# Kernel tuning notes

Hardware: AMD Instinct MI355X
Metric: run time of the kernel (lower is better)

The kernel has to match this reference:

```python
import jax, jax.numpy as jnp
import numpy as np

D_MODEL = 1024
NUM_HEADS = 16
D_K = D_MODEL // NUM_HEADS


def setup_inputs() -> dict:
    key = jax.random.key(0)
    ks = jax.random.split(key, 9)
    s = 1.0 / np.sqrt(D_MODEL)
    return {
        "z": jax.random.normal(ks[0], (4, 2048, D_MODEL), dtype=jnp.float32),
        "Wq": jax.random.uniform(ks[1], (D_MODEL, D_MODEL), jnp.float32, -s, s),
        "bq": jax.random.uniform(ks[2], (D_MODEL,), jnp.float32, -s, s),
        "Wk": jax.random.uniform(ks[3], (D_MODEL, D_MODEL), jnp.float32, -s, s),
        "bk": jax.random.uniform(ks[4], (D_MODEL,), jnp.float32, -s, s),
        "Wv": jax.random.uniform(ks[5], (D_MODEL, D_MODEL), jnp.float32, -s, s),
        "bv": jax.random.uniform(ks[6], (D_MODEL,), jnp.float32, -s, s),
        "Wo": jax.random.uniform(ks[7], (D_MODEL, D_MODEL), jnp.float32, -s, s),
        "bo": jax.random.uniform(ks[8], (D_MODEL,), jnp.float32, -s, s),
    }


def reference(z, Wq, bq, Wk, bk, Wv, bv, Wo, bo):
    B, S, _ = z.shape
    # project and split heads: [B, H, S, d_k]
    def proj(W, b):
        return (z @ W.T + b).reshape(B, S, NUM_HEADS, D_K).transpose(0, 2, 1, 3)
    Q, K, V = proj(Wq, bq), proj(Wk, bk), proj(Wv, bv)
    scale = 1.0 / np.sqrt(D_K)
    scores = jnp.einsum('bhqd,bhkd->bhqk', Q, K) * scale
    probs = jax.nn.softmax(scores, axis=-1)
    ctx = jnp.einsum('bhqk,bhkd->bhqd', probs, V)
    ctx = ctx.transpose(0, 2, 1, 3).reshape(B, S, D_MODEL)
    return ctx @ Wo.T + bo
```

## Files before the change

### kernel.cpp

```cpp
#include <hip/hip_runtime.h>
#include <stdint.h>

#define D_MODEL 1024
#define NHEAD 16
#define DKH 64
#define BATCH 4
#define SEQ 2048
#define M_ROWS (BATCH*SEQ)
#define NBH (BATCH*NHEAD)

typedef float f32x4 __attribute__((ext_vector_type(4)));
typedef __bf16 bf16x8 __attribute__((ext_vector_type(8)));
typedef __bf16 bf16x4v __attribute__((ext_vector_type(4)));
typedef short short4v __attribute__((ext_vector_type(4)));

__device__ __forceinline__ unsigned short f2bf(float x) {
    __bf16 b = (__bf16)x;
    return __builtin_bit_cast(unsigned short, b);
}

#define GLL(gsrc, ldst) \
    __builtin_amdgcn_global_load_lds((const __attribute__((address_space(1))) void*)(gsrc), \
                                     (__attribute__((address_space(3))) void*)(ldst), 16, 0, 0)

__global__ __launch_bounds__(256) void k_convert(
    const float* __restrict__ z,  const float* __restrict__ wq,
    const float* __restrict__ wk, const float* __restrict__ wv,
    const float* __restrict__ wo,
    const float* __restrict__ bq, const float* __restrict__ bk,
    const float* __restrict__ bv,
    unsigned short* __restrict__ zb, unsigned short* __restrict__ wqkv,
    unsigned short* __restrict__ wob, float* __restrict__ biasf)
{
    int i = blockIdx.x * 256 + threadIdx.x;
    {
        float4 v = ((const float4*)z)[i];
        ushort4 o; o.x = f2bf(v.x); o.y = f2bf(v.y); o.z = f2bf(v.z); o.w = f2bf(v.w);
        ((ushort4*)zb)[i] = o;
    }
    if (i < 262144) {
        float4 v;
        ushort4 o;
        v = ((const float4*)wq)[i];
        o.x=f2bf(v.x); o.y=f2bf(v.y); o.z=f2bf(v.z); o.w=f2bf(v.w);
        ((ushort4*)wqkv)[i] = o;
        v = ((const float4*)wk)[i];
        o.x=f2bf(v.x); o.y=f2bf(v.y); o.z=f2bf(v.z); o.w=f2bf(v.w);
        ((ushort4*)wqkv)[262144 + i] = o;
        v = ((const float4*)wv)[i];
        o.x=f2bf(v.x); o.y=f2bf(v.y); o.z=f2bf(v.z); o.w=f2bf(v.w);
        ((ushort4*)wqkv)[524288 + i] = o;
        v = ((const float4*)wo)[i];
        o.x=f2bf(v.x); o.y=f2bf(v.y); o.z=f2bf(v.z); o.w=f2bf(v.w);
        ((ushort4*)wob)[i] = o;
    }
    if (i < 1024) {
        biasf[i]        = bq[i];
        biasf[1024 + i] = bk[i];
        biasf[2048 + i] = bv[i];
    }
}

__global__ __launch_bounds__(256) void k_gemm_qkv(
    const unsigned short* __restrict__ A,
    const unsigned short* __restrict__ Bw,
    const float* __restrict__ biasf,
    unsigned short* __restrict__ qb, unsigned short* __restrict__ kb,
    unsigned short* __restrict__ vtb)
{
    __shared__ unsigned short lds_a[128 * 32];
    __shared__ unsigned short lds_b[128 * 32];

    const int NT = 3072 / 128;
    int bid = blockIdx.x;
    int tn = bid % NT, tm = bid / NT;
    int m0 = tm * 128, n0 = tn * 128;
    int tid = threadIdx.x, wid = tid >> 6, lane = tid & 63;
    int wm = wid >> 1, wn = wid & 1;

    f32x4 acc[4][4] = {};

    int srow = lane >> 2;
    int scol = (lane & 3) * 8;

    for (int kt = 0; kt < 32; ++kt) {
        int k0 = kt * 32;
#pragma unroll
        for (int i = 0; i < 2; ++i) {
            int rb = (wid * 2 + i) * 16;
            GLL(A  + (size_t)(m0 + rb + srow) * 1024 + k0 + scol, lds_a + rb * 32);
            GLL(Bw + (size_t)(n0 + rb + srow) * 1024 + k0 + scol, lds_b + rb * 32);
        }
        __syncthreads();
        bf16x8 af[4], bfr[4];
#pragma unroll
        for (int i = 0; i < 4; ++i)
            af[i] = *(const bf16x8*)(lds_a + (wm * 64 + i * 16 + (lane & 15)) * 32 + (lane >> 4) * 8);
#pragma unroll
        for (int j = 0; j < 4; ++j)
            bfr[j] = *(const bf16x8*)(lds_b + (wn * 64 + j * 16 + (lane & 15)) * 32 + (lane >> 4) * 8);
#pragma unroll
        for (int i = 0; i < 4; ++i)
#pragma unroll
            for (int j = 0; j < 4; ++j)
                acc[i][j] = __builtin_amdgcn_mfma_f32_16x16x32_bf16(af[i], bfr[j], acc[i][j], 0, 0, 0);
        __syncthreads();
    }

    const float QSC = 0.18033688011112042f;
    int t = n0 >> 10;
#pragma unroll
    for (int j = 0; j < 4; ++j) {
        int col = n0 + wn * 64 + j * 16 + (lane & 15);
        float bias = biasf[col];
        int d  = col & 1023;
        int h  = d >> 6;
        int dk = d & 63;
#pragma unroll
        for (int i = 0; i < 4; ++i) {
#pragma unroll
            for (int r = 0; r < 4; ++r) {
                int row = m0 + wm * 64 + i * 16 + (lane >> 4) * 4 + r;
                float v = acc[i][j][r] + bias;
                if (t == 0) v *= QSC;
                unsigned short bv16 = f2bf(v);
                int b_ = row >> 11, s_ = row & 2047;
                int bh = b_ * NHEAD + h;
                if (t == 0)      qb[((size_t)bh * SEQ + s_) * DKH + dk] = bv16;
                else if (t == 1) kb[((size_t)bh * SEQ + s_) * DKH + dk] = bv16;
                else             vtb[((size_t)bh * DKH + dk) * SEQ + s_] = bv16;
            }
        }
    }
}

__device__ __forceinline__ void stage_kv(
    const unsigned short* __restrict__ kb, const unsigned short* __restrict__ vtb,
    unsigned short* lk, unsigned short* lv,
    int bh, int t, int wid, int srow8, int sc)
{
#pragma unroll
    for (int i = 0; i < 2; ++i) {
        int rb = wid * 16 + i * 8;
        int row = rb + srow8;
        int cs = (sc ^ (row & 7)) * 8;
        GLL(kb  + ((size_t)bh * SEQ + t * 64 + row) * DKH + cs, lk + rb * 64);
        GLL(vtb + ((size_t)bh * DKH + row) * SEQ + t * 64 + cs, lv + rb * 64);
    }
}

__global__ __launch_bounds__(256) void k_attn(
    const unsigned short* __restrict__ qg,
    const unsigned short* __restrict__ kb,
    const unsigned short* __restrict__ vtb,
    unsigned short* __restrict__ ctxb)
{
    __shared__ unsigned short lds_k[2][64 * 64];
    __shared__ unsigned short lds_v[2][64 * 64];

    int bid = blockIdx.x;
    int x = bid & 7, li = bid >> 3;
    int bh = x * 8 + (li >> 4);
    int qt = li & 15;

    int tid = threadIdx.x, wid = tid >> 6, lane = tid & 63;
    int lq = lane & 15, g = lane >> 4;
    int srow8 = lane >> 3, sc = lane & 7;

    bf16x8 aq[2][2];
    {
        const unsigned short* qp = qg + ((size_t)bh * SEQ + qt * 128 + wid * 32 + lq) * DKH + g * 8;
        aq[0][0] = *(const bf16x8*)(qp);
        aq[0][1] = *(const bf16x8*)(qp + 32);
        aq[1][0] = *(const bf16x8*)(qp + 16 * DKH);
        aq[1][1] = *(const bf16x8*)(qp + 16 * DKH + 32);
    }

    float lsum[2] = { 0.f, 0.f };
    f32x4 oacc[2][4] = {};

    stage_kv(kb, vtb, &lds_k[0][0], &lds_v[0][0], bh, 0, wid, srow8, sc);

    for (int kt = 0; kt < 32; ++kt) {
        int cur = kt & 1;
        if (kt < 31) {
            stage_kv(kb, vtb, &lds_k[cur ^ 1][0], &lds_v[cur ^ 1][0], bh, kt + 1, wid, srow8, sc);
            asm volatile("s_waitcnt vmcnt(4)" ::: "memory");
        } else {
            asm volatile("s_waitcnt vmcnt(0)" ::: "memory");
        }
        __builtin_amdgcn_s_barrier();

        f32x4 st[2][4] = {};
#pragma unroll
        for (int kk = 0; kk < 2; ++kk) {
            bf16x8 kf[4];
#pragma unroll
            for (int jb = 0; jb < 4; ++jb) {
                int row = jb * 16 + lq;
                int c = kk * 4 + g;
                kf[jb] = *(const bf16x8*)(&lds_k[cur][row * 64 + ((c ^ (row & 7)) * 8)]);
            }
#pragma unroll
            for (int jb = 0; jb < 4; ++jb)
#pragma unroll
                for (int q = 0; q < 2; ++q)
                    st[q][jb] = __builtin_amdgcn_mfma_f32_16x16x32_bf16(kf[jb], aq[q][kk], st[q][jb], 0, 0, 0);
        }

        short4v w[2][4];
#pragma unroll
        for (int q = 0; q < 2; ++q) {
#pragma unroll
            for (int jb = 0; jb < 4; ++jb) {
                float p0 = __builtin_amdgcn_exp2f(st[q][jb][0]);
                float p1 = __builtin_amdgcn_exp2f(st[q][jb][1]);
                float p2 = __builtin_amdgcn_exp2f(st[q][jb][2]);
                float p3 = __builtin_amdgcn_exp2f(st[q][jb][3]);
                lsum[q] += (p0 + p1) + (p2 + p3);
                bf16x4v pb;
                pb[0] = (__bf16)p0; pb[1] = (__bf16)p1; pb[2] = (__bf16)p2; pb[3] = (__bf16)p3;
                w[q][jb] = __builtin_bit_cast(short4v, pb);
            }
        }

#pragma unroll
        for (int dj = 0; dj < 4; ++dj) {
            int row = dj * 16 + lq;
            int rx = row & 7;
#pragma unroll
            for (int jb = 0; jb < 4; ++jb) {
                int c = jb * 2 + (g >> 1);
                short4v vf = *(const short4v*)(&lds_v[cur][row * 64 + ((c ^ rx) * 8) + (g & 1) * 4]);
#pragma unroll
                for (int q = 0; q < 2; ++q)
                    oacc[q][dj] = __builtin_amdgcn_mfma_f32_16x16x16bf16_1k(vf, w[q][jb], oacc[q][dj], 0, 0, 0);
            }
        }
        __builtin_amdgcn_s_barrier();
    }

    int b_ = bh >> 4, h = bh & 15;
#pragma unroll
    for (int q = 0; q < 2; ++q) {
        float s = lsum[q];
        s += __shfl_xor(s, 16);
        s += __shfl_xor(s, 32);
        float inv = 1.0f / s;
        int s_ = qt * 128 + wid * 32 + q * 16 + lq;
        unsigned short* op = ctxb + (((size_t)b_ * SEQ + s_) * NHEAD + h) * DKH;
#pragma unroll
        for (int dj = 0; dj < 4; ++dj) {
#pragma unroll
            for (int t = 0; t < 2; ++t) {
                unsigned short e0 = f2bf(oacc[q][dj][2 * t]     * inv);
                unsigned short e1 = f2bf(oacc[q][dj][2 * t + 1] * inv);
                unsigned int u = ((unsigned int)e1 << 16) | (unsigned int)e0;
                *(unsigned int*)(op + dj * 16 + 4 * g + 2 * t) = u;
            }
        }
    }
}

__global__ __launch_bounds__(256) void k_gemm_out(
    const unsigned short* __restrict__ A,
    const unsigned short* __restrict__ Bw,
    const float* __restrict__ bo,
    float* __restrict__ out)
{
    __shared__ unsigned short lds_a[128 * 32];
    __shared__ unsigned short lds_b[128 * 32];

    const int NT = 1024 / 128;
    int bid = blockIdx.x;
    int tn = bid % NT, tm = bid / NT;
    int m0 = tm * 128, n0 = tn * 128;
    int tid = threadIdx.x, wid = tid >> 6, lane = tid & 63;
    int wm = wid >> 1, wn = wid & 1;

    f32x4 acc[4][4] = {};

    int srow = lane >> 2;
    int scol = (lane & 3) * 8;

    for (int kt = 0; kt < 32; ++kt) {
        int k0 = kt * 32;
#pragma unroll
        for (int i = 0; i < 2; ++i) {
            int rb = (wid * 2 + i) * 16;
            GLL(A  + (size_t)(m0 + rb + srow) * 1024 + k0 + scol, lds_a + rb * 32);
            GLL(Bw + (size_t)(n0 + rb + srow) * 1024 + k0 + scol, lds_b + rb * 32);
        }
        __syncthreads();
        bf16x8 af[4], bfr[4];
#pragma unroll
        for (int i = 0; i < 4; ++i)
            af[i] = *(const bf16x8*)(lds_a + (wm * 64 + i * 16 + (lane & 15)) * 32 + (lane >> 4) * 8);
#pragma unroll
        for (int j = 0; j < 4; ++j)
            bfr[j] = *(const bf16x8*)(lds_b + (wn * 64 + j * 16 + (lane & 15)) * 32 + (lane >> 4) * 8);
#pragma unroll
        for (int i = 0; i < 4; ++i)
#pragma unroll
            for (int j = 0; j < 4; ++j)
                acc[i][j] = __builtin_amdgcn_mfma_f32_16x16x32_bf16(af[i], bfr[j], acc[i][j], 0, 0, 0);
        __syncthreads();
    }

#pragma unroll
    for (int j = 0; j < 4; ++j) {
        int col = n0 + wn * 64 + j * 16 + (lane & 15);
        float bias = bo[col];
#pragma unroll
        for (int i = 0; i < 4; ++i) {
#pragma unroll
            for (int r = 0; r < 4; ++r) {
                int row = m0 + wm * 64 + i * 16 + (lane >> 4) * 4 + r;
                out[(size_t)row * 1024 + col] = acc[i][j][r] + bias;
            }
        }
    }
}

extern "C" void kernel_launch(void* const* d_in, const int* in_sizes, int n_in,
                              void* d_out, int out_size, void* d_ws, size_t ws_size,
                              hipStream_t stream)
{
    const float* z  = (const float*)d_in[0];
    const float* Wq = (const float*)d_in[1];
    const float* bq = (const float*)d_in[2];
    const float* Wk = (const float*)d_in[3];
    const float* bk = (const float*)d_in[4];
    const float* Wv = (const float*)d_in[5];
    const float* bv = (const float*)d_in[6];
    const float* Wo = (const float*)d_in[7];
    const float* bo = (const float*)d_in[8];
    float* out = (float*)d_out;

    char* ws = (char*)d_ws;
    unsigned short* zb   = (unsigned short*)(ws);
    unsigned short* ctxb = (unsigned short*)(ws);
    unsigned short* wqkv = (unsigned short*)(ws + (16ull << 20));
    unsigned short* wob  = (unsigned short*)(ws + (22ull << 20));
    float*          biasf= (float*)(ws + (24ull << 20));
    unsigned short* qb   = (unsigned short*)(ws + (25ull << 20));
    unsigned short* kb   = (unsigned short*)(ws + (41ull << 20));
    unsigned short* vtb  = (unsigned short*)(ws + (57ull << 20));

    k_convert<<<8192, 256, 0, stream>>>(z, Wq, Wk, Wv, Wo, bq, bk, bv, zb, wqkv, wob, biasf);
    k_gemm_qkv<<<64 * 24, 256, 0, stream>>>(zb, wqkv, biasf, qb, kb, vtb);
    k_attn<<<NBH * 16, 256, 0, stream>>>(qb, kb, vtb, ctxb);
    k_gemm_out<<<64 * 8, 256, 0, stream>>>(ctxb, wob, bo, out);
}
```

Baseline: 244.1 us.

## Stage V through registers with 4-element XOR swizzle and add MFMA priority hints

V tiles are no longer copied straight to LDS with global_load_lds. Each thread now loads them into registers early in the iteration and writes them to LDS after the PV MFMAs, using a 4-element-granularity XOR swizzle meant to cut LDS bank conflicts on the 4-wide V fragment reads. The loop also drops to a single barrier per iteration and wraps the MFMA sections in s_setprio to favour matrix issue. This costs extra VGPRs for the in-flight V data and a full vmcnt(0) wait before the LDS write.

```diff
diff --git a/kernel.cpp b/kernel.cpp
--- a/kernel.cpp
+++ b/kernel.cpp
@@ -13,6 +13,8 @@
 typedef __bf16 bf16x8 __attribute__((ext_vector_type(8)));
 typedef __bf16 bf16x4v __attribute__((ext_vector_type(4)));
 typedef short short4v __attribute__((ext_vector_type(4)));
+typedef int int2v __attribute__((ext_vector_type(2)));
+typedef int int4v __attribute__((ext_vector_type(4)));
 
 __device__ __forceinline__ unsigned short f2bf(float x) {
     __bf16 b = (__bf16)x;
@@ -134,19 +136,37 @@
     }
 }
 
-__device__ __forceinline__ void stage_kv(
-    const unsigned short* __restrict__ kb, const unsigned short* __restrict__ vtb,
-    unsigned short* lk, unsigned short* lv,
-    int bh, int t, int wid, int srow8, int sc)
+__device__ __forceinline__ void stage_k(
+    const unsigned short* __restrict__ kb,
+    unsigned short* lk, int bh, int t, int wid, int srow8, int sc)
 {
 #pragma unroll
     for (int i = 0; i < 2; ++i) {
         int rb = wid * 16 + i * 8;
         int row = rb + srow8;
         int cs = (sc ^ (row & 7)) * 8;
-        GLL(kb  + ((size_t)bh * SEQ + t * 64 + row) * DKH + cs, lk + rb * 64);
-        GLL(vtb + ((size_t)bh * DKH + row) * SEQ + t * 64 + cs, lv + rb * 64);
-    }
+        GLL(kb + ((size_t)bh * SEQ + t * 64 + row) * DKH + cs, lk + rb * 64);
+    }
+}
+
+__device__ __forceinline__ void vload(
+    const unsigned short* __restrict__ vtb, int bh, int t, int vrow, int vseg,
+    int4v& r0, int4v& r1)
+{
+    const unsigned short* p = vtb + ((size_t)bh * DKH + vrow) * SEQ + t * 64 + vseg * 16;
+    r0 = *(const int4v*)(p);
+    r1 = *(const int4v*)(p + 8);
+}
+
+__device__ __forceinline__ void vwrite(
+    unsigned short* lv, int vrow, int vseg, const int4v& r0, const int4v& r1)
+{
+    int rx = vrow & 15;
+    unsigned short* base = lv + vrow * 64;
+    *(int2v*)(base + (((vseg * 4 + 0) ^ rx) * 4)) = (int2v){ r0[0], r0[1] };
+    *(int2v*)(base + (((vseg * 4 + 1) ^ rx) * 4)) = (int2v){ r0[2], r0[3] };
+    *(int2v*)(base + (((vseg * 4 + 2) ^ rx) * 4)) = (int2v){ r1[0], r1[1] };
+    *(int2v*)(base + (((vseg * 4 + 3) ^ rx) * 4)) = (int2v){ r1[2], r1[3] };
 }
 
 __global__ __launch_bounds__(256) void k_attn(
@@ -166,6 +186,7 @@
     int tid = threadIdx.x, wid = tid >> 6, lane = tid & 63;
     int lq = lane & 15, g = lane >> 4;
     int srow8 = lane >> 3, sc = lane & 7;
+    int vrow = wid * 16 + (lane >> 2), vseg = lane & 3;
 
     bf16x8 aq[2][2];
     {
@@ -179,19 +200,25 @@
     float lsum[2] = { 0.f, 0.f };
     f32x4 oacc[2][4] = {};
 
-    stage_kv(kb, vtb, &lds_k[0][0], &lds_v[0][0], bh, 0, wid, srow8, sc);
+    int4v vr0, vr1;
+
+    stage_k(kb, &lds_k[0][0], bh, 0, wid, srow8, sc);
+    vload(vtb, bh, 0, vrow, vseg, vr0, vr1);
+    asm volatile("s_waitcnt vmcnt(0)" ::: "memory");
+    vwrite(&lds_v[0][0], vrow, vseg, vr0, vr1);
+    asm volatile("s_waitcnt lgkmcnt(0)" ::: "memory");
+    __builtin_amdgcn_sched_barrier(0);
+    __builtin_amdgcn_s_barrier();
 
     for (int kt = 0; kt < 32; ++kt) {
         int cur = kt & 1;
         if (kt < 31) {
-            stage_kv(kb, vtb, &lds_k[cur ^ 1][0], &lds_v[cur ^ 1][0], bh, kt + 1, wid, srow8, sc);
-            asm volatile("s_waitcnt vmcnt(4)" ::: "memory");
-        } else {
-            asm volatile("s_waitcnt vmcnt(0)" ::: "memory");
-        }
-        __builtin_amdgcn_s_barrier();
+            stage_k(kb, &lds_k[cur ^ 1][0], bh, kt + 1, wid, srow8, sc);
+            vload(vtb, bh, kt + 1, vrow, vseg, vr0, vr1);
+        }
 
         f32x4 st[2][4] = {};
+        __builtin_amdgcn_s_setprio(1);
 #pragma unroll
         for (int kk = 0; kk < 2; ++kk) {
             bf16x8 kf[4];
@@ -207,6 +234,7 @@
                 for (int q = 0; q < 2; ++q)
                     st[q][jb] = __builtin_amdgcn_mfma_f32_16x16x32_bf16(kf[jb], aq[q][kk], st[q][jb], 0, 0, 0);
         }
+        __builtin_amdgcn_s_setprio(0);
 
         short4v w[2][4];
 #pragma unroll
@@ -224,19 +252,26 @@
             }
         }
 
+        __builtin_amdgcn_s_setprio(1);
 #pragma unroll
         for (int dj = 0; dj < 4; ++dj) {
-            int row = dj * 16 + lq;
-            int rx = row & 7;
+            int rbase = (dj * 16 + lq) * 64;
 #pragma unroll
             for (int jb = 0; jb < 4; ++jb) {
-                int c = jb * 2 + (g >> 1);
-                short4v vf = *(const short4v*)(&lds_v[cur][row * 64 + ((c ^ rx) * 8) + (g & 1) * 4]);
+                short4v vf = *(const short4v*)(&lds_v[cur][rbase + (((jb * 4 + g) ^ lq) * 4)]);
 #pragma unroll
                 for (int q = 0; q < 2; ++q)
                     oacc[q][dj] = __builtin_amdgcn_mfma_f32_16x16x16bf16_1k(vf, w[q][jb], oacc[q][dj], 0, 0, 0);
             }
         }
+        __builtin_amdgcn_s_setprio(0);
+
+        if (kt < 31) {
+            asm volatile("s_waitcnt vmcnt(0)" ::: "memory");
+            vwrite(&lds_v[cur ^ 1][0], vrow, vseg, vr0, vr1);
+        }
+        asm volatile("s_waitcnt lgkmcnt(0)" ::: "memory");
+        __builtin_amdgcn_sched_barrier(0);
         __builtin_amdgcn_s_barrier();
     }
 
```

New measurement: 239.4 us. Within noise of the previous version (-1.9%).
